# Kernel tuning notes

Measured on AMD Instinct MI355X. Metric: run time of the kernel, lower is better.

The kernel has to match this reference:

```python
import jax, jax.numpy as jnp
import numpy as np

B, C, H, W = 4, 256, 32, 32
N_HEADS, N_GROUPS = 8, 4
HEAD_C = C // N_HEADS            # 32
GROUP_C = C // N_GROUPS          # 64
GROUP_HEADS = N_HEADS // N_GROUPS  # 2
OFFSET_RANGE_FACTOR = 4.0
SCALE = HEAD_C ** -0.5
EPS = 1e-5


def grid_sample(img, grid):
    """Bilinear grid_sample, align_corners=True, zeros padding.
    img: (N, Ch, Hi, Wi); grid: (N, Hg, Wg, 2) with (x, y) in [-1, 1]."""
    N, Ch, Hi, Wi = img.shape
    x = (grid[..., 0] + 1.0) * 0.5 * (Wi - 1)
    y = (grid[..., 1] + 1.0) * 0.5 * (Hi - 1)
    x0 = jnp.floor(x); y0 = jnp.floor(y)
    x1 = x0 + 1.0; y1 = y0 + 1.0
    wx1 = x - x0; wx0 = 1.0 - wx1
    wy1 = y - y0; wy0 = 1.0 - wy1
    img_flat = img.reshape(N, Ch, Hi * Wi)

    def corner(xi, yi, w):
        valid = (xi >= 0) & (xi <= Wi - 1) & (yi >= 0) & (yi <= Hi - 1)
        xc = jnp.clip(xi, 0, Wi - 1).astype(jnp.int32)
        yc = jnp.clip(yi, 0, Hi - 1).astype(jnp.int32)
        idx = yc * Wi + xc  # (N, Hg, Wg)
        vals = jax.vmap(lambda im, ix: im[:, ix])(img_flat, idx)  # (N, Ch, Hg, Wg)
        return vals * (w * valid)[:, None, :, :]

    return (corner(x0, y0, wx0 * wy0) + corner(x1, y0, wx1 * wy0)
            + corner(x0, y1, wx0 * wy1) + corner(x1, y1, wx1 * wy1))


def setup_inputs() -> dict:
    key = jax.random.key(0)
    ks = jax.random.split(key, 12)
    s = C ** -0.5
    return {
        "q_feat": jax.random.normal(ks[0], (B, C, H, W), jnp.float32),
        "kv_feat": jax.random.normal(ks[1], (B, C, H, W), jnp.float32),
        "Wq": jax.random.normal(ks[2], (C, C), jnp.float32) * s,
        "bq": jnp.zeros((C,), jnp.float32),
        "Wk": jax.random.normal(ks[3], (C, C), jnp.float32) * s,
        "bk": jnp.zeros((C,), jnp.float32),
        "Wv": jax.random.normal(ks[4], (C, C), jnp.float32) * s,
        "bv": jnp.zeros((C,), jnp.float32),
        "Wo": jax.random.normal(ks[5], (C, C), jnp.float32) * s,
        "bo": jnp.zeros((C,), jnp.float32),
        "off_dw_w": jax.random.normal(ks[6], (GROUP_C, 1, 3, 3), jnp.float32) / 3.0,
        "off_dw_b": jnp.zeros((GROUP_C,), jnp.float32),
        "off_ln_w": jnp.ones((GROUP_C,), jnp.float32),
        "off_ln_b": jnp.zeros((GROUP_C,), jnp.float32),
        "off_pw_w": jax.random.normal(ks[7], (2, GROUP_C), jnp.float32) * GROUP_C ** -0.5,
        "rpe_table": jax.random.normal(ks[8], (N_HEADS, 2 * H - 1, 2 * W - 1), jnp.float32) * 0.01,
    }


def reference(q_feat, kv_feat, Wq, bq, Wk, bk, Wv, bv, Wo, bo,
              off_dw_w, off_dw_b, off_ln_w, off_ln_b, off_pw_w, rpe_table):
    Bg = B * N_GROUPS
    n = H * W
    # q projection (1x1 conv)
    q = jnp.einsum('oi,bihw->bohw', Wq, q_feat) + bq[:, None, None]
    # offset network on grouped q
    q_off = q.reshape(Bg, GROUP_C, H, W)
    x = jax.lax.conv_general_dilated(q_off, off_dw_w, (1, 1), ((1, 1), (1, 1)),
                                     feature_group_count=GROUP_C,
                                     dimension_numbers=('NCHW', 'OIHW', 'NCHW'))
    x = x + off_dw_b[:, None, None]
    mu = x.mean(1, keepdims=True)
    var = x.var(1, keepdims=True)
    x = (x - mu) / jnp.sqrt(var + EPS) * off_ln_w[:, None, None] + off_ln_b[:, None, None]
    x = jax.nn.gelu(x, approximate=False)
    offset = jnp.einsum('oc,bchw->bohw', off_pw_w, x)  # (Bg, 2, H, W), (y, x)
    off_range = jnp.array([1.0 / (H - 1), 1.0 / (W - 1)], jnp.float32).reshape(1, 2, 1, 1)
    offset = jnp.tanh(offset) * off_range * OFFSET_RANGE_FACTOR
    offset = offset.transpose(0, 2, 3, 1)  # (Bg, H, W, 2)
    # reference points in [-1, 1]
    ref_y = (jnp.linspace(0.5, H - 0.5, H) / (H - 1.0)) * 2.0 - 1.0
    ref_x = (jnp.linspace(0.5, W - 0.5, W) / (W - 1.0)) * 2.0 - 1.0
    ref = jnp.stack(jnp.meshgrid(ref_y, ref_x, indexing='ij'), -1)  # (H, W, 2)
    pos = offset + ref[None]  # (Bg, H, W, 2), (y, x), no clamp (offset_range_factor >= 0)
    # deformable sampling of kv features
    kv_g = kv_feat.reshape(Bg, GROUP_C, H, W)
    x_sampled = grid_sample(kv_g, pos[..., ::-1]).reshape(B, C, n)
    k = jnp.einsum('oi,bin->bon', Wk, x_sampled) + bk[:, None]
    v = jnp.einsum('oi,bin->bon', Wv, x_sampled) + bv[:, None]
    qf = q.reshape(B, N_HEADS, HEAD_C, n)
    kf = k.reshape(B, N_HEADS, HEAD_C, n)
    vf = v.reshape(B, N_HEADS, HEAD_C, n)
    attn = jnp.einsum('bhcm,bhcn->bhmn', qf, kf) * SCALE
    # relative-position bias via bilinear sampling of rpe table
    gy = (jnp.arange(H, dtype=jnp.float32) / (H - 1.0)) * 2.0 - 1.0
    gx = (jnp.arange(W, dtype=jnp.float32) / (W - 1.0)) * 2.0 - 1.0
    q_grid = jnp.stack(jnp.meshgrid(gy, gx, indexing='ij'), -1).reshape(n, 2)
    pos_flat = pos.reshape(Bg, n, 2)
    disp = (q_grid[None, :, None, :] - pos_flat[:, None, :, :]) * 0.5  # (Bg, m, n, 2)
    rpe = jnp.broadcast_to(
        rpe_table.reshape(1, N_GROUPS, GROUP_HEADS, 2 * H - 1, 2 * W - 1),
        (B, N_GROUPS, GROUP_HEADS, 2 * H - 1, 2 * W - 1)
    ).reshape(Bg, GROUP_HEADS, 2 * H - 1, 2 * W - 1)
    bias = grid_sample(rpe, disp[..., ::-1])  # (Bg, GROUP_HEADS, m, n)
    attn = attn + bias.reshape(B, N_HEADS, n, n)
    attn = jax.nn.softmax(attn, axis=-1)
    out = jnp.einsum('bhmn,bhcn->bhcm', attn, vf).reshape(B, C, H, W)
    out = jnp.einsum('oi,bihw->bohw', Wo, out) + bo[:, None, None]
    return out
```

## Files before the change

kernel.cpp:

```cpp
#include <hip/hip_runtime.h>
#include <hip/hip_bf16.h>
#include <math.h>
#include <stdint.h>

#define BB 4
#define CC 256
#define HH 32
#define WW 32
#define NPIX 1024
#define NHEADS 8
#define NGROUPS 4
#define HEADC 32
#define GROUPC 64
#define BG 16
#define RPE_N 3969
#define SCALE_QK 0.17677669529663687f
#define LN_EPS 1e-5f

#define W_Q   0
#define W_POS 1048576
#define W_XS  1081344
#define W_KT  2129920
#define W_VV  2654208
#define W_AO  3178496

using frag  = __attribute__((ext_vector_type(8))) short;
using f32x4 = __attribute__((ext_vector_type(4))) float;

struct InPtrs { const void* p[16]; };

__device__ __forceinline__ float tof(float x){ return x; }
__device__ __forceinline__ float tof(__hip_bfloat16 x){ return __bfloat162float(x); }
__device__ __forceinline__ short bfs(float v) {
  __hip_bfloat16 h = __float2bfloat16(v);
  return *(short*)&h;
}
__device__ __forceinline__ bool is_f32(const void* lnw) {
  return *(const unsigned int*)lnw == 0x3F800000u;
}
__device__ __forceinline__ float ldm(const void* p, size_t i, bool f32m) {
  return f32m ? ((const float*)p)[i] : __bfloat162float(((const __hip_bfloat16*)p)[i]);
}
__device__ __forceinline__ float lof(uint32_t g){ return __uint_as_float(g << 16); }
__device__ __forceinline__ float hif(uint32_t g){ return __uint_as_float(g & 0xffff0000u); }

template<int TM>
__device__ __forceinline__ void gemm_body(const void* xsrc, bool xf32,
    const void* wraw, bool wf32, int b, int o0, int mb,
    short* Bs, f32x4* acc) {
  const int tid = threadIdx.x;
  const int wave = tid >> 6, lane = tid & 63, quad = lane >> 4, l15 = lane & 15;
  const int og = wave & 3, mh = wave >> 2;
  const int MS = TM >> 5;
  const int NE = TM >> 4;

  size_t gbase[NE];
  int lbase[NE];
  #pragma unroll
  for (int it = 0; it < NE; ++it) {
    int i = tid + 512 * it;
    int mm = i & (TM - 1), kk = i / TM;
    gbase[it] = ((size_t)(b * CC + kk)) * NPIX + mb + mm;
    lbase[it] = mm * 72 + ((((kk >> 3) ^ (mm & 3))) << 4) + (kk & 7);
  }

  float v[NE];
  #pragma unroll
  for (int it = 0; it < NE; ++it)
    v[it] = xf32 ? ((const float*)xsrc)[gbase[it]]
                 : __bfloat162float(((const __hip_bfloat16*)xsrc)[gbase[it]]);

  for (int s = 0; s < 8; ++s) {
    short* buf = Bs + (s & 1) * (TM * 72);
    #pragma unroll
    for (int it = 0; it < NE; ++it) {
      __hip_bfloat16 h = __float2bfloat16(v[it]);
      buf[lbase[it]] = *(short*)&h;
      buf[lbase[it] + 8] = bfs(v[it] - __bfloat162float(h));
    }
    if (s < 7) {
      size_t koff = (size_t)(s + 1) * 32 * NPIX;
      #pragma unroll
      for (int it = 0; it < NE; ++it)
        v[it] = xf32 ? ((const float*)xsrc)[gbase[it] + koff]
                     : __bfloat162float(((const __hip_bfloat16*)xsrc)[gbase[it] + koff]);
    }
    const int k0 = s * 32;
    size_t wofs = (size_t)(o0 + og * 16 + l15) * CC + k0 + quad * 8;
    float wv[8];
    if (wf32) {
      float4 wa = *(const float4*)((const float*)wraw + wofs);
      float4 wb = *(const float4*)((const float*)wraw + wofs + 4);
      wv[0]=wa.x; wv[1]=wa.y; wv[2]=wa.z; wv[3]=wa.w;
      wv[4]=wb.x; wv[5]=wb.y; wv[6]=wb.z; wv[7]=wb.w;
    } else {
      const __hip_bfloat16* wp = (const __hip_bfloat16*)wraw + wofs;
      #pragma unroll
      for (int j = 0; j < 8; ++j) wv[j] = __bfloat162float(wp[j]);
    }
    frag wh, wl;
    #pragma unroll
    for (int j = 0; j < 8; ++j) {
      __hip_bfloat16 h = __float2bfloat16(wv[j]);
      wh[j] = *(short*)&h;
      wl[j] = bfs(wv[j] - __bfloat162float(h));
    }
    __syncthreads();
    #pragma unroll
    for (int ms = 0; ms < MS; ++ms) {
      int ml = mh * (TM >> 1) + ms * 16 + l15;
      const short* bp = buf + ml * 72 + ((quad ^ (ml & 3)) << 4);
      frag bh = *(const frag*)bp;
      frag bl = *(const frag*)(bp + 8);
      acc[ms] = __builtin_amdgcn_mfma_f32_16x16x32_bf16(wh, bh, acc[ms], 0, 0, 0);
      acc[ms] = __builtin_amdgcn_mfma_f32_16x16x32_bf16(wh, bl, acc[ms], 0, 0, 0);
      acc[ms] = __builtin_amdgcn_mfma_f32_16x16x32_bf16(wl, bh, acc[ms], 0, 0, 0);
    }
  }
}

__global__ __launch_bounds__(512)
void qproj_kernel(InPtrs ip, float* __restrict__ q) {
  __shared__ __align__(16) short Bs[2 * 32 * 72];
  bool f32m = is_f32(ip.p[12]);
  int mb = blockIdx.x * 32, o0 = blockIdx.y * 64, b = blockIdx.z;
  int tid = threadIdx.x;
  int wave = tid >> 6, lane = tid & 63, quad = lane >> 4, l15 = lane & 15;
  f32x4 acc[1] = {{0.f,0.f,0.f,0.f}};
  gemm_body<32>(ip.p[0], f32m, ip.p[2], f32m, b, o0, mb, Bs, acc);
  int og = wave & 3, mh = wave >> 2;
  int od = o0 + og * 16 + quad * 4;
  float bv[4];
  #pragma unroll
  for (int r = 0; r < 4; ++r) bv[r] = ldm(ip.p[3], od + r, f32m);
  int m = mb + mh * 16 + l15;
  #pragma unroll
  for (int r = 0; r < 4; ++r)
    q[(size_t)(b * CC + od + r) * NPIX + m] = acc[0][r] + bv[r];
}

__global__ __launch_bounds__(512)
void kvproj_kernel(InPtrs ip, const float* __restrict__ xs,
                   __hip_bfloat16* __restrict__ kT, __hip_bfloat16* __restrict__ vbf) {
  __shared__ __align__(16) char arena[2 * 64 * 72 * 2];
  bool f32m = is_f32(ip.p[12]);
  int mt = blockIdx.x, ot = blockIdx.y, b = blockIdx.z;
  int mb = mt * 64;
  bool isV = (ot >= 4);
  int o0 = (ot & 3) * 64;
  const void* wraw = isV ? ip.p[6] : ip.p[4];
  const void* braw = isV ? ip.p[7] : ip.p[5];
  int tid = threadIdx.x;
  int wave = tid >> 6, lane = tid & 63, quad = lane >> 4, l15 = lane & 15;
  f32x4 acc[2] = {{0.f,0.f,0.f,0.f},{0.f,0.f,0.f,0.f}};
  gemm_body<64>(xs, true, wraw, f32m, b, o0, mb, (short*)arena, acc);
  int og = wave & 3, mh = wave >> 2;
  int od = o0 + og * 16 + quad * 4;
  float bv[4];
  #pragma unroll
  for (int r = 0; r < 4; ++r) bv[r] = ldm(braw, od + r, f32m);
  if (isV) {
    #pragma unroll
    for (int ms = 0; ms < 2; ++ms) {
      int m = mb + mh * 32 + ms * 16 + l15;
      #pragma unroll
      for (int r = 0; r < 4; ++r)
        vbf[(size_t)(b * CC + od + r) * NPIX + m] = __float2bfloat16(acc[ms][r] + bv[r]);
    }
  } else {
    __syncthreads();
    float* Ds = (float*)arena;
    #pragma unroll
    for (int ms = 0; ms < 2; ++ms) {
      int ml = mh * 32 + ms * 16 + l15;
      #pragma unroll
      for (int r = 0; r < 4; ++r)
        Ds[(og * 16 + quad * 4 + r) * 65 + ml] = acc[ms][r] + bv[r];
    }
    __syncthreads();
    int ot4 = ot & 3;
    {
      int q2 = tid;
      int m = q2 >> 3, cc = q2 & 7;
      __hip_bfloat16 t8[8];
      #pragma unroll
      for (int j = 0; j < 8; ++j)
        t8[j] = __float2bfloat16(Ds[(cc * 8 + j) * 65 + m]);
      int h = ot4 * 2 + (cc >> 2);
      size_t addr = ((size_t)(b * NHEADS + h) * NPIX + mb + m) * HEADC + (cc & 3) * 8;
      *(uint4*)((short*)kT + addr) = *(const uint4*)t8;
    }
  }
}

__global__ __launch_bounds__(512)
void oproj_kernel(InPtrs ip, const float* __restrict__ ao, void* __restrict__ out) {
  __shared__ __align__(16) short Bs[2 * 32 * 72];
  bool f32m = is_f32(ip.p[12]);
  int mb = blockIdx.x * 32, o0 = blockIdx.y * 64, b = blockIdx.z;
  int tid = threadIdx.x;
  int wave = tid >> 6, lane = tid & 63, quad = lane >> 4, l15 = lane & 15;
  f32x4 acc[1] = {{0.f,0.f,0.f,0.f}};
  gemm_body<32>(ao, true, ip.p[8], f32m, b, o0, mb, Bs, acc);
  int og = wave & 3, mh = wave >> 2;
  int od = o0 + og * 16 + quad * 4;
  float bv[4];
  #pragma unroll
  for (int r = 0; r < 4; ++r) bv[r] = ldm(ip.p[9], od + r, f32m);
  int m = mb + mh * 16 + l15;
  #pragma unroll
  for (int r = 0; r < 4; ++r) {
    float val = acc[0][r] + bv[r];
    size_t idx = (size_t)(b * CC + od + r) * NPIX + m;
    if (f32m) ((float*)out)[idx] = val;
    else      ((__hip_bfloat16*)out)[idx] = __float2bfloat16(val);
  }
}

template<typename T>
__device__ __forceinline__ float tap4(const T* __restrict__ img,
                                      int x0, int y0,
                                      float wx0, float wx1, float wy0, float wy1) {
  bool xv0 = (x0 >= 0) & (x0 < WW);
  bool xv1 = (x0 >= -1) & (x0 < WW - 1);
  bool yv0 = (y0 >= 0) & (y0 < HH);
  bool yv1 = (y0 >= -1) & (y0 < HH - 1);
  float acc = 0.0f;
  if (xv0 & yv0) acc += wx0 * wy0 * tof(img[y0 * WW + x0]);
  if (xv1 & yv0) acc += wx1 * wy0 * tof(img[y0 * WW + x0 + 1]);
  if (xv0 & yv1) acc += wx0 * wy1 * tof(img[(y0 + 1) * WW + x0]);
  if (xv1 & yv1) acc += wx1 * wy1 * tof(img[(y0 + 1) * WW + x0 + 1]);
  return acc;
}

__global__ __launch_bounds__(512)
void offsample_kernel(InPtrs ip, const float* __restrict__ q,
                      float* __restrict__ pos, float* __restrict__ xs) {
  __shared__ float qs[128][65];
  __shared__ float posl[2][64];
  bool f32m = is_f32(ip.p[12]);
  int blk = blockIdx.x;
  int hh2 = blk & 15, bg = blk >> 4;
  int b = bg >> 2, g = bg & 3;
  int tid = threadIdx.x;
  const float* qg = q + (size_t)(b * CC + g * GROUPC) * NPIX;
  #pragma unroll
  for (int k = 0; k < 16; ++k) {
    int idx = tid + 512 * k;
    int ww = idx & 31, c = (idx >> 5) & 63, r3 = idx >> 11;
    int yy = hh2 * 2 - 1 + r3;
    float v = (yy >= 0 && yy < HH) ? qg[(size_t)c * NPIX + yy * WW + ww] : 0.0f;
    qs[r3 * 32 + ww][c] = v;
  }
  __syncthreads();
  {
    int wave = tid >> 6, c = tid & 63;
    int lr = wave >> 2, w4 = wave & 3;
    float wdw[9];
    #pragma unroll
    for (int j = 0; j < 9; ++j) wdw[j] = ldm(ip.p[10], c * 9 + j, f32m);
    float bdw = ldm(ip.p[11], c, f32m);
    float lnw = ldm(ip.p[12], c, f32m), lnb = ldm(ip.p[13], c, f32m);
    float pwy = ldm(ip.p[14], c, f32m), pwx = ldm(ip.p[14], GROUPC + c, f32m);

    for (int p8 = 0; p8 < 8; ++p8) {
      int ww = w4 * 8 + p8;
      float x = bdw;
      #pragma unroll
      for (int dy = 0; dy < 3; ++dy)
        #pragma unroll
        for (int dx = 0; dx < 3; ++dx) {
          int xx = ww + dx - 1;
          if (xx >= 0 && xx < WW) x += wdw[dy * 3 + dx] * qs[(lr + dy) * 32 + xx][c];
        }
      float s = x, s2 = x * x;
      #pragma unroll
      for (int off = 32; off > 0; off >>= 1) {
        s  += __shfl_xor(s,  off);
        s2 += __shfl_xor(s2, off);
      }
      float mu  = s * (1.0f / 64.0f);
      float var = s2 * (1.0f / 64.0f) - mu * mu;
      float xn = (x - mu) * (1.0f / sqrtf(var + LN_EPS)) * lnw + lnb;
      float ge = 0.5f * xn * (1.0f + erff(xn * 0.70710678118654752f));
      float oy = pwy * ge, ox = pwx * ge;
      #pragma unroll
      for (int off = 32; off > 0; off >>= 1) {
        oy += __shfl_xor(oy, off);
        ox += __shfl_xor(ox, off);
      }
      if (c == 0) {
        int hh = hh2 * 2 + lr;
        float fy = tanhf(oy) * (4.0f / 31.0f);
        float fx = tanhf(ox) * (4.0f / 31.0f);
        float ry = ((0.5f + (float)hh) / 31.0f) * 2.0f - 1.0f;
        float rx = ((0.5f + (float)ww) / 31.0f) * 2.0f - 1.0f;
        float py = fy + ry, px = fx + rx;
        int m = hh * 32 + ww;
        pos[((size_t)bg * NPIX + m) * 2 + 0] = py;
        pos[((size_t)bg * NPIX + m) * 2 + 1] = px;
        posl[lr][ww * 2 + 0] = py;
        posl[lr][ww * 2 + 1] = px;
      }
    }
  }
  __syncthreads();
  #pragma unroll
  for (int k = 0; k < 8; ++k) {
    int s = tid + 512 * k;
    int ww = s & 31, lr = (s >> 5) & 1, c = s >> 6;
    float py = posl[lr][ww * 2 + 0], px = posl[lr][ww * 2 + 1];
    float xi = (px + 1.0f) * 15.5f, yi = (py + 1.0f) * 15.5f;
    float x0f = floorf(xi), y0f = floorf(yi);
    float wx1 = xi - x0f, wx0 = 1.0f - wx1;
    float wy1 = yi - y0f, wy0 = 1.0f - wy1;
    int x0 = (int)x0f, y0 = (int)y0f;
    size_t img_off = (size_t)(b * CC + g * GROUPC + c) * NPIX;
    float acc;
    if (f32m) acc = tap4((const float*)ip.p[1] + img_off, x0, y0, wx0, wx1, wy0, wy1);
    else      acc = tap4((const __hip_bfloat16*)ip.p[1] + img_off, x0, y0, wx0, wx1, wy0, wy1);
    xs[img_off + (hh2 * 2 + lr) * 32 + ww] = acc;
  }
}

__global__ __launch_bounds__(512, 3)
void attn_mfma_kernel(InPtrs ip, const float* __restrict__ q,
                      const __hip_bfloat16* __restrict__ kT,
                      const __hip_bfloat16* __restrict__ vbf,
                      const float* __restrict__ pos, float* __restrict__ ao) {
  __shared__ uint32_t Du[68 * 69];
  __shared__ __align__(16) __hip_bfloat16 Pw[8][16][72];
  __shared__ __align__(16) __hip_bfloat16 qA[16][40];
  __shared__ float redmax[8 * 16];
  __shared__ float redsum[8 * 16];

  bool f32m = is_f32(ip.p[12]);
  int bh = blockIdx.x;
  int b = bh >> 3, h = bh & 7;
  int m0 = blockIdx.y * 16;
  int tid = threadIdx.x;
  int bg = b * 4 + (h >> 1);

  size_t slice = (size_t)(b * CC + h * HEADC) * NPIX;
  const short* kTb = (const short*)kT + (size_t)bh * NPIX * HEADC;
  const short* vb = (const short*)vbf + slice;
  const float* qb = q + slice;
  const float* posb = pos + (size_t)bg * NPIX * 2;

  {
    const size_t rbase = (size_t)h * RPE_N;
    for (int i = tid; i < 68 * 69; i += 512) {
      int r = i / 69, c = i - r * 69;
      int y = r - 3, x = c - 3;
      bool yv = (y >= 0) & (y < 63);
      float va = (yv & (x >= 0) & (x < 63)) ? ldm(ip.p[15], rbase + y * 63 + x, f32m) : 0.0f;
      float vb2 = (yv & (x >= -1) & (x < 62)) ? ldm(ip.p[15], rbase + y * 63 + x + 1, f32m) : 0.0f;
      __hip_bfloat16 ha = __float2bfloat16(va), hb = __float2bfloat16(vb2);
      Du[i] = (uint32_t)*(unsigned short*)&ha | ((uint32_t)*(unsigned short*)&hb << 16);
    }
  }
  {
    int r = tid & 15, c = tid >> 4;
    qA[r][c] = __float2bfloat16(qb[(size_t)c * NPIX + m0 + r] * SCALE_QK);
  }
  __syncthreads();

  int wave = tid >> 6, lane = tid & 63;
  int quad = lane >> 4, l15 = lane & 15;
  int nbase = wave * 128;

  frag aq = *(const frag*)&qA[l15][quad * 8];
  float ybase = 31.0f + 15.5f * ((float)(m0 >> 5) * (2.0f / 31.0f) - 1.0f);
  float xbase0 = 31.0f + 15.5f * ((float)(m0 & 31) * (2.0f / 31.0f) - 1.0f);

  float pm[4], ps[4];
  f32x4 acc0 = {0.f,0.f,0.f,0.f}, acc1 = {0.f,0.f,0.f,0.f};
  #pragma unroll
  for (int reg = 0; reg < 4; ++reg) { pm[reg] = -1e30f; ps[reg] = 0.0f; }

  #pragma unroll
  for (int half = 0; half < 2; ++half) {
    int hbase = nbase + half * 64;
    float sreg[4][4];
    #pragma unroll
    for (int t8 = 0; t8 < 4; ++t8) {
      int n = hbase + t8 * 16 + l15;
      frag bk = *(const frag*)(kTb + (size_t)n * HEADC + quad * 8);
      f32x4 d = __builtin_amdgcn_mfma_f32_16x16x32_bf16(aq, bk, (f32x4){0.f,0.f,0.f,0.f}, 0, 0, 0);
      float2 pp = *(const float2*)(posb + 2 * n);
      float yi = ybase - 15.5f * pp.x;
      float y0f = floorf(yi);
      float wy1 = yi - y0f, wy0 = 1.0f - wy1;
      float xi0 = xbase0 - 15.5f * pp.y;
      float x0f = floorf(xi0);
      float wx1 = xi0 - x0f, wx0 = 1.0f - wx1;
      int row = (int)y0f + 3;
      int col = (int)x0f + 3 + quad * 4;
      const uint32_t* Dp = Du + row * 69 + col;
      uint32_t g0 = Dp[0],  g1 = Dp[2],  g2 = Dp[4];
      uint32_t h0 = Dp[69], h1 = Dp[71], h2 = Dp[73];
      float u[5];
      u[0] = wy0 * lof(g0) + wy1 * lof(h0);
      u[1] = wy0 * hif(g0) + wy1 * hif(h0);
      u[2] = wy0 * lof(g1) + wy1 * lof(h1);
      u[3] = wy0 * hif(g1) + wy1 * hif(h1);
      u[4] = wy0 * lof(g2) + wy1 * lof(h2);
      #pragma unroll
      for (int reg = 0; reg < 4; ++reg)
        sreg[t8][reg] = d[reg] + wx0 * u[reg] + wx1 * u[reg + 1];
    }
    #pragma unroll
    for (int reg = 0; reg < 4; ++reg) {
      float m = fmaxf(fmaxf(sreg[0][reg], sreg[1][reg]),
                      fmaxf(sreg[2][reg], sreg[3][reg]));
      m = fmaxf(m, __shfl_xor(m, 1));
      m = fmaxf(m, __shfl_xor(m, 2));
      m = fmaxf(m, __shfl_xor(m, 4));
      m = fmaxf(m, __shfl_xor(m, 8));
      float newm = fmaxf(pm[reg], m);
      float sc = __expf(pm[reg] - newm);
      pm[reg] = newm;
      ps[reg] *= sc;
      acc0[reg] *= sc;
      acc1[reg] *= sc;
    }
    #pragma unroll
    for (int t8 = 0; t8 < 4; ++t8) {
      #pragma unroll
      for (int reg = 0; reg < 4; ++reg) {
        float p = __expf(sreg[t8][reg] - pm[reg]);
        Pw[wave][quad * 4 + reg][t8 * 16 + l15] = __float2bfloat16(p);
        ps[reg] += p;
      }
    }
    #pragma unroll
    for (int ks = 0; ks < 2; ++ks) {
      int koff = hbase + ks * 32 + quad * 8;
      frag ap = *(const frag*)&Pw[wave][l15][ks * 32 + quad * 8];
      frag bv0 = *(const frag*)(vb + (size_t)l15 * NPIX + koff);
      frag bv1 = *(const frag*)(vb + (size_t)(16 + l15) * NPIX + koff);
      acc0 = __builtin_amdgcn_mfma_f32_16x16x32_bf16(ap, bv0, acc0, 0, 0, 0);
      acc1 = __builtin_amdgcn_mfma_f32_16x16x32_bf16(ap, bv1, acc1, 0, 0, 0);
    }
  }

  #pragma unroll
  for (int reg = 0; reg < 4; ++reg) {
    ps[reg] += __shfl_xor(ps[reg], 1);
    ps[reg] += __shfl_xor(ps[reg], 2);
    ps[reg] += __shfl_xor(ps[reg], 4);
    ps[reg] += __shfl_xor(ps[reg], 8);
  }
  if (l15 == 0) {
    #pragma unroll
    for (int reg = 0; reg < 4; ++reg) {
      redmax[wave * 16 + quad * 4 + reg] = pm[reg];
      redsum[wave * 16 + quad * 4 + reg] = ps[reg];
    }
  }
  __syncthreads();

  float* part = (float*)&Pw[0][0][0];
  {
    int e0 = (0 * 16 + l15) * 16 + quad * 4;
    int e1 = (1 * 16 + l15) * 16 + quad * 4;
    #pragma unroll
    for (int reg = 0; reg < 4; ++reg) {
      part[wave * 512 + e0 + reg] = acc0[reg];
      part[wave * 512 + e1 + reg] = acc1[reg];
    }
  }
  __syncthreads();

  {
    int c = tid >> 4, r = tid & 15;
    float M = -1e30f;
    #pragma unroll
    for (int w2 = 0; w2 < 8; ++w2) M = fmaxf(M, redmax[w2 * 16 + r]);
    float num = 0.0f, den = 0.0f;
    #pragma unroll
    for (int w2 = 0; w2 < 8; ++w2) {
      float sc = __expf(redmax[w2 * 16 + r] - M);
      num += part[w2 * 512 + tid] * sc;
      den += redsum[w2 * 16 + r] * sc;
    }
    ao[slice + (size_t)c * NPIX + m0 + r] = num / den;
  }
}

extern "C" void kernel_launch(void* const* d_in, const int* in_sizes, int n_in,
                              void* d_out, int out_size, void* d_ws, size_t ws_size,
                              hipStream_t stream) {
  float* ws  = (float*)d_ws;
  float* q   = ws + W_Q;
  float* pos = ws + W_POS;
  float* xs  = ws + W_XS;
  __hip_bfloat16* kT  = (__hip_bfloat16*)(ws + W_KT);
  __hip_bfloat16* vbf = (__hip_bfloat16*)(ws + W_VV);
  float* ao  = ws + W_AO;

  InPtrs ip;
  for (int i = 0; i < 16; ++i) ip.p[i] = d_in[i];

  qproj_kernel<<<dim3(32, 4, 4), 512, 0, stream>>>(ip, q);
  offsample_kernel<<<BG * 16, 512, 0, stream>>>(ip, q, pos, xs);
  kvproj_kernel<<<dim3(16, 8, 4), 512, 0, stream>>>(ip, xs, kT, vbf);
  attn_mfma_kernel<<<dim3(32, 64), 512, 0, stream>>>(ip, q, kT, vbf, pos, ao);
  oproj_kernel<<<dim3(32, 4, 4), 512, 0, stream>>>(ip, ao, d_out);
}
```

Before: 193.9 us.

## Precompute packed RPE table and split bf16 weights in a prep kernel

Adds a prep kernel that builds the padded, bf16-pair-packed RPE table per head and the hi/lo bf16 splits of all four projection weights into workspace once per call. The attention kernel then copies the packed table into shared memory with vector loads instead of rebuilding it in each of its many blocks. The GEMM kernels load the pre-split fragments instead of converting weights inline. The offset/sample kernel is also re-tiled to one row per block, doubling its grid. The cost is an extra kernel launch and extra workspace traffic.

```diff
diff --git a/kernel.cpp b/kernel.cpp
--- a/kernel.cpp
+++ b/kernel.cpp
@@ -23,6 +23,10 @@
 #define W_KT  2129920
 #define W_VV  2654208
 #define W_AO  3178496
+#define W_RPE 4227072
+#define W_WSP 4264608
+
+#define RPE_PACKED 4692
 
 using frag  = __attribute__((ext_vector_type(8))) short;
 using f32x4 = __attribute__((ext_vector_type(4))) float;
@@ -44,9 +48,46 @@
 __device__ __forceinline__ float lof(uint32_t g){ return __uint_as_float(g << 16); }
 __device__ __forceinline__ float hif(uint32_t g){ return __uint_as_float(g & 0xffff0000u); }
 
+__global__ __launch_bounds__(512)
+void prep_kernel(InPtrs ip, uint32_t* __restrict__ rpeg,
+                 unsigned short* __restrict__ wsp) {
+  bool f32m = is_f32(ip.p[12]);
+  int blk = blockIdx.x;
+  int tid = threadIdx.x;
+  if (blk < 8) {
+    int h = blk;
+    const size_t rbase = (size_t)h * RPE_N;
+    uint32_t* dst = rpeg + (size_t)h * RPE_PACKED;
+    for (int i = tid; i < 68 * 69; i += 512) {
+      int r = i / 69, c = i - r * 69;
+      int y = r - 3, x = c - 3;
+      bool yv = (y >= 0) & (y < 63);
+      float va = (yv & (x >= 0) & (x < 63)) ? ldm(ip.p[15], rbase + y * 63 + x, f32m) : 0.0f;
+      float vb2 = (yv & (x >= -1) & (x < 62)) ? ldm(ip.p[15], rbase + y * 63 + x + 1, f32m) : 0.0f;
+      __hip_bfloat16 ha = __float2bfloat16(va), hb = __float2bfloat16(vb2);
+      dst[i] = (uint32_t)*(unsigned short*)&ha | ((uint32_t)*(unsigned short*)&hb << 16);
+    }
+  } else {
+    int wb = blk - 8;
+    const void* srcs[4] = { ip.p[2], ip.p[4], ip.p[6], ip.p[8] };
+    int idx0 = wb * 4096 + tid * 8;
+    int m = idx0 >> 16, e0 = idx0 & 65535;
+    const void* src = srcs[m];
+    unsigned short* hi = wsp + (size_t)m * 131072;
+    unsigned short* lo = hi + 65536;
+    #pragma unroll
+    for (int j = 0; j < 8; ++j) {
+      float w = ldm(src, e0 + j, f32m);
+      __hip_bfloat16 h = __float2bfloat16(w);
+      hi[e0 + j] = *(unsigned short*)&h;
+      lo[e0 + j] = (unsigned short)bfs(w - __bfloat162float(h));
+    }
+  }
+}
+
 template<int TM>
 __device__ __forceinline__ void gemm_body(const void* xsrc, bool xf32,
-    const void* wraw, bool wf32, int b, int o0, int mb,
+    const unsigned short* __restrict__ wsp, int b, int o0, int mb,
     short* Bs, f32x4* acc) {
   const int tid = threadIdx.x;
   const int wave = tid >> 6, lane = tid & 63, quad = lane >> 4, l15 = lane & 15;
@@ -87,24 +128,8 @@
     }
     const int k0 = s * 32;
     size_t wofs = (size_t)(o0 + og * 16 + l15) * CC + k0 + quad * 8;
-    float wv[8];
-    if (wf32) {
-      float4 wa = *(const float4*)((const float*)wraw + wofs);
-      float4 wb = *(const float4*)((const float*)wraw + wofs + 4);
-      wv[0]=wa.x; wv[1]=wa.y; wv[2]=wa.z; wv[3]=wa.w;
-      wv[4]=wb.x; wv[5]=wb.y; wv[6]=wb.z; wv[7]=wb.w;
-    } else {
-      const __hip_bfloat16* wp = (const __hip_bfloat16*)wraw + wofs;
-      #pragma unroll
-      for (int j = 0; j < 8; ++j) wv[j] = __bfloat162float(wp[j]);
-    }
-    frag wh, wl;
-    #pragma unroll
-    for (int j = 0; j < 8; ++j) {
-      __hip_bfloat16 h = __float2bfloat16(wv[j]);
-      wh[j] = *(short*)&h;
-      wl[j] = bfs(wv[j] - __bfloat162float(h));
-    }
+    frag wh = *(const frag*)(wsp + wofs);
+    frag wl = *(const frag*)(wsp + 65536 + wofs);
     __syncthreads();
     #pragma unroll
     for (int ms = 0; ms < MS; ++ms) {
@@ -120,14 +145,15 @@
 }
 
 __global__ __launch_bounds__(512)
-void qproj_kernel(InPtrs ip, float* __restrict__ q) {
+void qproj_kernel(InPtrs ip, const unsigned short* __restrict__ wsp,
+                  float* __restrict__ q) {
   __shared__ __align__(16) short Bs[2 * 32 * 72];
   bool f32m = is_f32(ip.p[12]);
   int mb = blockIdx.x * 32, o0 = blockIdx.y * 64, b = blockIdx.z;
   int tid = threadIdx.x;
   int wave = tid >> 6, lane = tid & 63, quad = lane >> 4, l15 = lane & 15;
   f32x4 acc[1] = {{0.f,0.f,0.f,0.f}};
-  gemm_body<32>(ip.p[0], f32m, ip.p[2], f32m, b, o0, mb, Bs, acc);
+  gemm_body<32>(ip.p[0], f32m, wsp, b, o0, mb, Bs, acc);
   int og = wave & 3, mh = wave >> 2;
   int od = o0 + og * 16 + quad * 4;
   float bv[4];
@@ -140,7 +166,8 @@
 }
 
 __global__ __launch_bounds__(512)
-void kvproj_kernel(InPtrs ip, const float* __restrict__ xs,
+void kvproj_kernel(InPtrs ip, const unsigned short* __restrict__ wspal,
+                   const float* __restrict__ xs,
                    __hip_bfloat16* __restrict__ kT, __hip_bfloat16* __restrict__ vbf) {
   __shared__ __align__(16) char arena[2 * 64 * 72 * 2];
   bool f32m = is_f32(ip.p[12]);
@@ -148,12 +175,12 @@
   int mb = mt * 64;
   bool isV = (ot >= 4);
   int o0 = (ot & 3) * 64;
-  const void* wraw = isV ? ip.p[6] : ip.p[4];
+  const unsigned short* wsp = wspal + (size_t)(isV ? 2 : 1) * 131072;
   const void* braw = isV ? ip.p[7] : ip.p[5];
   int tid = threadIdx.x;
   int wave = tid >> 6, lane = tid & 63, quad = lane >> 4, l15 = lane & 15;
   f32x4 acc[2] = {{0.f,0.f,0.f,0.f},{0.f,0.f,0.f,0.f}};
-  gemm_body<64>(xs, true, wraw, f32m, b, o0, mb, (short*)arena, acc);
+  gemm_body<64>(xs, true, wsp, b, o0, mb, (short*)arena, acc);
   int og = wave & 3, mh = wave >> 2;
   int od = o0 + og * 16 + quad * 4;
   float bv[4];
@@ -194,14 +221,15 @@
 }
 
 __global__ __launch_bounds__(512)
-void oproj_kernel(InPtrs ip, const float* __restrict__ ao, void* __restrict__ out) {
+void oproj_kernel(InPtrs ip, const unsigned short* __restrict__ wsp,
+                  const float* __restrict__ ao, void* __restrict__ out) {
   __shared__ __align__(16) short Bs[2 * 32 * 72];
   bool f32m = is_f32(ip.p[12]);
   int mb = blockIdx.x * 32, o0 = blockIdx.y * 64, b = blockIdx.z;
   int tid = threadIdx.x;
   int wave = tid >> 6, lane = tid & 63, quad = lane >> 4, l15 = lane & 15;
   f32x4 acc[1] = {{0.f,0.f,0.f,0.f}};
-  gemm_body<32>(ao, true, ip.p[8], f32m, b, o0, mb, Bs, acc);
+  gemm_body<32>(ao, true, wsp, b, o0, mb, Bs, acc);
   int og = wave & 3, mh = wave >> 2;
   int od = o0 + og * 16 + quad * 4;
   float bv[4];
@@ -236,26 +264,25 @@
 __global__ __launch_bounds__(512)
 void offsample_kernel(InPtrs ip, const float* __restrict__ q,
                       float* __restrict__ pos, float* __restrict__ xs) {
-  __shared__ float qs[128][65];
-  __shared__ float posl[2][64];
+  __shared__ float qs[96][65];
+  __shared__ float posl[64];
   bool f32m = is_f32(ip.p[12]);
   int blk = blockIdx.x;
-  int hh2 = blk & 15, bg = blk >> 4;
+  int hh = blk & 31, bg = blk >> 5;
   int b = bg >> 2, g = bg & 3;
   int tid = threadIdx.x;
   const float* qg = q + (size_t)(b * CC + g * GROUPC) * NPIX;
   #pragma unroll
-  for (int k = 0; k < 16; ++k) {
+  for (int k = 0; k < 12; ++k) {
     int idx = tid + 512 * k;
     int ww = idx & 31, c = (idx >> 5) & 63, r3 = idx >> 11;
-    int yy = hh2 * 2 - 1 + r3;
+    int yy = hh - 1 + r3;
     float v = (yy >= 0 && yy < HH) ? qg[(size_t)c * NPIX + yy * WW + ww] : 0.0f;
     qs[r3 * 32 + ww][c] = v;
   }
   __syncthreads();
   {
     int wave = tid >> 6, c = tid & 63;
-    int lr = wave >> 2, w4 = wave & 3;
     float wdw[9];
     #pragma unroll
     for (int j = 0; j < 9; ++j) wdw[j] = ldm(ip.p[10], c * 9 + j, f32m);
@@ -263,15 +290,15 @@
     float lnw = ldm(ip.p[12], c, f32m), lnb = ldm(ip.p[13], c, f32m);
     float pwy = ldm(ip.p[14], c, f32m), pwx = ldm(ip.p[14], GROUPC + c, f32m);
 
-    for (int p8 = 0; p8 < 8; ++p8) {
-      int ww = w4 * 8 + p8;
+    for (int p4 = 0; p4 < 4; ++p4) {
+      int ww = wave * 4 + p4;
       float x = bdw;
       #pragma unroll
       for (int dy = 0; dy < 3; ++dy)
         #pragma unroll
         for (int dx = 0; dx < 3; ++dx) {
           int xx = ww + dx - 1;
-          if (xx >= 0 && xx < WW) x += wdw[dy * 3 + dx] * qs[(lr + dy) * 32 + xx][c];
+          if (xx >= 0 && xx < WW) x += wdw[dy * 3 + dx] * qs[dy * 32 + xx][c];
         }
       float s = x, s2 = x * x;
       #pragma unroll
@@ -290,7 +317,6 @@
         ox += __shfl_xor(ox, off);
       }
       if (c == 0) {
-        int hh = hh2 * 2 + lr;
         float fy = tanhf(oy) * (4.0f / 31.0f);
         float fx = tanhf(ox) * (4.0f / 31.0f);
         float ry = ((0.5f + (float)hh) / 31.0f) * 2.0f - 1.0f;
@@ -299,17 +325,17 @@
         int m = hh * 32 + ww;
         pos[((size_t)bg * NPIX + m) * 2 + 0] = py;
         pos[((size_t)bg * NPIX + m) * 2 + 1] = px;
-        posl[lr][ww * 2 + 0] = py;
-        posl[lr][ww * 2 + 1] = px;
+        posl[ww * 2 + 0] = py;
+        posl[ww * 2 + 1] = px;
       }
     }
   }
   __syncthreads();
   #pragma unroll
-  for (int k = 0; k < 8; ++k) {
+  for (int k = 0; k < 4; ++k) {
     int s = tid + 512 * k;
-    int ww = s & 31, lr = (s >> 5) & 1, c = s >> 6;
-    float py = posl[lr][ww * 2 + 0], px = posl[lr][ww * 2 + 1];
+    int ww = s & 31, c = (s >> 5) & 63;
+    float py = posl[ww * 2 + 0], px = posl[ww * 2 + 1];
     float xi = (px + 1.0f) * 15.5f, yi = (py + 1.0f) * 15.5f;
     float x0f = floorf(xi), y0f = floorf(yi);
     float wx1 = xi - x0f, wx0 = 1.0f - wx1;
@@ -319,22 +345,22 @@
     float acc;
     if (f32m) acc = tap4((const float*)ip.p[1] + img_off, x0, y0, wx0, wx1, wy0, wy1);
     else      acc = tap4((const __hip_bfloat16*)ip.p[1] + img_off, x0, y0, wx0, wx1, wy0, wy1);
-    xs[img_off + (hh2 * 2 + lr) * 32 + ww] = acc;
+    xs[img_off + hh * 32 + ww] = acc;
   }
 }
 
 __global__ __launch_bounds__(512, 3)
-void attn_mfma_kernel(InPtrs ip, const float* __restrict__ q,
+void attn_mfma_kernel(InPtrs ip, const uint32_t* __restrict__ rpeg,
+                      const float* __restrict__ q,
                       const __hip_bfloat16* __restrict__ kT,
                       const __hip_bfloat16* __restrict__ vbf,
                       const float* __restrict__ pos, float* __restrict__ ao) {
-  __shared__ uint32_t Du[68 * 69];
+  __shared__ __align__(16) uint32_t Du[RPE_PACKED];
   __shared__ __align__(16) __hip_bfloat16 Pw[8][16][72];
   __shared__ __align__(16) __hip_bfloat16 qA[16][40];
   __shared__ float redmax[8 * 16];
   __shared__ float redsum[8 * 16];
 
-  bool f32m = is_f32(ip.p[12]);
   int bh = blockIdx.x;
   int b = bh >> 3, h = bh & 7;
   int m0 = blockIdx.y * 16;
@@ -348,16 +374,9 @@
   const float* posb = pos + (size_t)bg * NPIX * 2;
 
   {
-    const size_t rbase = (size_t)h * RPE_N;
-    for (int i = tid; i < 68 * 69; i += 512) {
-      int r = i / 69, c = i - r * 69;
-      int y = r - 3, x = c - 3;
-      bool yv = (y >= 0) & (y < 63);
-      float va = (yv & (x >= 0) & (x < 63)) ? ldm(ip.p[15], rbase + y * 63 + x, f32m) : 0.0f;
-      float vb2 = (yv & (x >= -1) & (x < 62)) ? ldm(ip.p[15], rbase + y * 63 + x + 1, f32m) : 0.0f;
-      __hip_bfloat16 ha = __float2bfloat16(va), hb = __float2bfloat16(vb2);
-      Du[i] = (uint32_t)*(unsigned short*)&ha | ((uint32_t)*(unsigned short*)&hb << 16);
-    }
+    const uint4* src = (const uint4*)(rpeg + (size_t)h * RPE_PACKED);
+    uint4* dst = (uint4*)Du;
+    for (int i = tid; i < 1173; i += 512) dst[i] = src[i];
   }
   {
     int r = tid & 15, c = tid >> 4;
@@ -498,13 +517,16 @@
   __hip_bfloat16* kT  = (__hip_bfloat16*)(ws + W_KT);
   __hip_bfloat16* vbf = (__hip_bfloat16*)(ws + W_VV);
   float* ao  = ws + W_AO;
+  uint32_t* rpeg = (uint32_t*)(ws + W_RPE);
+  unsigned short* wsp = (unsigned short*)(ws + W_WSP);
 
   InPtrs ip;
   for (int i = 0; i < 16; ++i) ip.p[i] = d_in[i];
 
-  qproj_kernel<<<dim3(32, 4, 4), 512, 0, stream>>>(ip, q);
-  offsample_kernel<<<BG * 16, 512, 0, stream>>>(ip, q, pos, xs);
-  kvproj_kernel<<<dim3(16, 8, 4), 512, 0, stream>>>(ip, xs, kT, vbf);
-  attn_mfma_kernel<<<dim3(32, 64), 512, 0, stream>>>(ip, q, kT, vbf, pos, ao);
-  oproj_kernel<<<dim3(32, 4, 4), 512, 0, stream>>>(ip, ao, d_out);
-}
+  prep_kernel<<<72, 512, 0, stream>>>(ip, rpeg, wsp);
+  qproj_kernel<<<dim3(32, 4, 4), 512, 0, stream>>>(ip, wsp, q);
+  offsample_kernel<<<BG * 32, 512, 0, stream>>>(ip, q, pos, xs);
+  kvproj_kernel<<<dim3(16, 8, 4), 512, 0, stream>>>(ip, wsp, xs, kT, vbf);
+  attn_mfma_kernel<<<dim3(32, 64), 512, 0, stream>>>(ip, rpeg, q, kT, vbf, pos, ao);
+  oproj_kernel<<<dim3(32, 4, 4), 512, 0, stream>>>(ip, wsp + (size_t)3 * 131072, ao, d_out);
+}
```

After: 180.0 us, median of 2. 7.1% less time.
